# Optimization experiments

Measured on AMD Instinct MI355X. Metric: run time of the kernel, lower is better.

Reference implementation:

```python
import jax, jax.numpy as jnp
import numpy as np
import math

D_MODEL = 32    # channels; expand=1 => d_inner == d_model
D_STATE = 8
D_CONV = 4
DT_RANK = math.ceil(D_MODEL / 16)  # 2


def _layernorm(x, g, b, eps=1e-5):
    m = jnp.mean(x, axis=-1, keepdims=True)
    v = jnp.var(x, axis=-1, keepdims=True)
    return (x - m) * jax.lax.rsqrt(v + eps) * g + b


def _causal_dwconv(x, w, b):
    # x: [B, D, L], w: [D, 1, K] depthwise causal conv (pad K-1 on the left)
    y = jax.lax.conv_general_dilated(
        x, w, window_strides=(1,), padding=[(D_CONV - 1, 0)],
        dimension_numbers=('NCH', 'OIH', 'NCH'),
        feature_group_count=x.shape[1])
    return y + b[None, :, None]


def _ssm_branch(xb, z, conv_w, conv_b, xproj_w, dtproj_w, dtproj_b, A_log, Dp):
    # One mamba_inner (no out_proj) branch. xb, z: [B, D, L]
    Bsz, Dd, L = xb.shape
    u = jax.nn.silu(_causal_dwconv(xb, conv_w, conv_b))              # [B,D,L]
    x_dbl = jnp.einsum('bdl,rd->blr', u, xproj_w)                    # [B,L,R+2N]
    dt = x_dbl[..., :DT_RANK]                                        # [B,L,R]
    Bm = x_dbl[..., DT_RANK:DT_RANK + D_STATE]                       # [B,L,N]
    Cm = x_dbl[..., DT_RANK + D_STATE:]                              # [B,L,N]
    delta = jax.nn.softplus(jnp.einsum('blr,dr->bld', dt, dtproj_w) + dtproj_b)  # [B,L,D]
    A = -jnp.exp(A_log)                                              # [D,N]

    def step(h, inp):
        d_l, u_l, B_l, C_l = inp   # [B,D], [B,D], [B,N], [B,N]
        dA = jnp.exp(d_l[..., None] * A)                             # [B,D,N]
        h = dA * h + (d_l * u_l)[..., None] * B_l[:, None, :]
        y = jnp.einsum('bdn,bn->bd', h, C_l)
        return h, y

    h0 = jnp.zeros((Bsz, Dd, D_STATE), dtype=xb.dtype)
    _, ys = jax.lax.scan(step, h0,
                         (delta.transpose(1, 0, 2), u.transpose(2, 0, 1),
                          Bm.transpose(1, 0, 2), Cm.transpose(1, 0, 2)))
    y = ys.transpose(1, 2, 0)                                        # [B,D,L]
    y = y + Dp[None, :, None] * u
    return y * jax.nn.silu(z)


def _forward(x, w1, b1, ln_g, ln_b, in_proj_w,
             conv_w_f, conv_b_f, xproj_w_f, dtproj_w_f, dtproj_b_f, A_log_f, D_f,
             conv_w_b, conv_b_b, xproj_w_b, dtproj_w_b, dtproj_b_b, A_log_b, D_b,
             norm_g, norm_b, out_proj_w, w2, b2):
    s = jnp.max(x, axis=(2, 3))                                      # AdaptiveMaxPool2d((1,1)) -> [B,L]
    h = s[..., None] * w1[None, None, :, 0] + b1                     # Linear(1, d_model) -> [B,L,D]
    h = _layernorm(h, ln_g, ln_b)
    # Mamba, bimamba v2
    xz = jnp.einsum('bld,ed->bel', h, in_proj_w)                     # [B,2D,L]
    x_f, z_f = jnp.split(xz, 2, axis=1)
    out_f = _ssm_branch(x_f, z_f, conv_w_f, conv_b_f, xproj_w_f,
                        dtproj_w_f, dtproj_b_f, A_log_f, D_f)
    xz_r = jnp.flip(xz, axis=-1)
    x_b, z_b = jnp.split(xz_r, 2, axis=1)
    out_b = _ssm_branch(x_b, z_b, conv_w_b, conv_b_b, xproj_w_b,
                        dtproj_w_b, dtproj_b_b, A_log_b, D_b)
    y = (out_f + jnp.flip(out_b, axis=-1)).transpose(0, 2, 1)        # [B,L,D]
    y = _layernorm(y, norm_g, norm_b) / 2.0                          # use_norm + if_devide_out
    y = jnp.einsum('bld,od->blo', y, out_proj_w)                     # out_proj -> [B,L,D]
    o = jnp.einsum('bld,od->blo', y, w2) + b2                        # Linear(d_model, 1) -> [B,L,1]
    return jax.nn.sigmoid(o)[..., None]                              # [B,L,1,1]


def setup_inputs() -> dict:
    key = jax.random.key(0)
    ks = jax.random.split(key, 16)
    B, Cin, H, W = 16, 128, 256, 256
    D, N, R = D_MODEL, D_STATE, DT_RANK

    def nrm(k, shp, s=0.2):
        return jax.random.normal(k, shp, dtype=jnp.float32) * s

    A_log_init = jnp.log(jnp.arange(1, N + 1, dtype=jnp.float32))[None, :] * jnp.ones((D, 1), jnp.float32)
    return dict(
        x=jax.random.normal(ks[0], (B, Cin, H, W), dtype=jnp.float32),
        w1=nrm(ks[1], (D, 1), 0.5), b1=nrm(ks[2], (D,), 0.1),
        ln_g=jnp.ones((D,), jnp.float32), ln_b=jnp.zeros((D,), jnp.float32),
        in_proj_w=nrm(ks[3], (2 * D, D)),
        conv_w_f=nrm(ks[4], (D, 1, D_CONV)), conv_b_f=nrm(ks[5], (D,), 0.1),
        xproj_w_f=nrm(ks[6], (R + 2 * N, D)),
        dtproj_w_f=nrm(ks[7], (D, R)), dtproj_b_f=nrm(ks[8], (D,), 0.1),
        A_log_f=A_log_init, D_f=jnp.ones((D,), jnp.float32),
        conv_w_b=nrm(ks[9], (D, 1, D_CONV)), conv_b_b=nrm(ks[10], (D,), 0.1),
        xproj_w_b=nrm(ks[11], (R + 2 * N, D)),
        dtproj_w_b=nrm(ks[12], (D, R)), dtproj_b_b=nrm(ks[13], (D,), 0.1),
        A_log_b=A_log_init, D_b=jnp.ones((D,), jnp.float32),
        norm_g=jnp.ones((D,), jnp.float32), norm_b=jnp.zeros((D,), jnp.float32),
        out_proj_w=nrm(ks[14], (D, D)),
        w2=nrm(ks[15], (1, D), 0.5), b2=jnp.zeros((1,), jnp.float32),
    )


def reference(x, w1, b1, ln_g, ln_b, in_proj_w,
              conv_w_f, conv_b_f, xproj_w_f, dtproj_w_f, dtproj_b_f, A_log_f, D_f,
              conv_w_b, conv_b_b, xproj_w_b, dtproj_w_b, dtproj_b_b, A_log_b, D_b,
              norm_g, norm_b, out_proj_w, w2, b2):
    return _forward(x, w1, b1, ln_g, ln_b, in_proj_w,
                    conv_w_f, conv_b_f, xproj_w_f, dtproj_w_f, dtproj_b_f, A_log_f, D_f,
                    conv_w_b, conv_b_b, xproj_w_b, dtproj_w_b, dtproj_b_b, A_log_b, D_b,
                    norm_g, norm_b, out_proj_w, w2, b2)
```

## Files before the change

kernel.cpp:

```cpp
#include <hip/hip_runtime.h>
#include <hip/hip_bf16.h>
#include <math.h>

#define B_SZ 16
#define L_SEQ 128
#define D_M 32
#define N_ST 8
#define HW 65536
#define NROWS (B_SZ * 128)
#define NCHUNK 2

typedef float vfloat4 __attribute__((ext_vector_type(4)));

__device__ float g_part[NROWS * NCHUNK];
__device__ float g_y0[B_SZ * D_M * L_SEQ];
__device__ float g_y1[B_SZ * D_M * L_SEQ];

__device__ __forceinline__ float silu_acc(float x) {
    return x / (1.f + expf(-x));
}
__device__ __forceinline__ float softplusf(float x) {
    return (x > 20.f) ? x : log1pf(expf(x));
}

__device__ __forceinline__ float sum8_dpp(float y) {
    float t;
    t = __int_as_float(__builtin_amdgcn_mov_dpp(__float_as_int(y), 0xB1, 0xF, 0xF, true));
    y += t;
    t = __int_as_float(__builtin_amdgcn_mov_dpp(__float_as_int(y), 0x4E, 0xF, 0xF, true));
    y += t;
    t = __int_as_float(__builtin_amdgcn_mov_dpp(__float_as_int(y), 0x141, 0xF, 0xF, true));
    y += t;
    return y;
}

__global__ __launch_bounds__(256) void kmax(const float* __restrict__ x) {
    const int blk = blockIdx.x;
    const vfloat4* __restrict__ p =
        reinterpret_cast<const vfloat4*>(x) + (size_t)blk * 8192;
    const int t = threadIdx.x;
    float m0 = -INFINITY, m1 = -INFINITY, m2 = -INFINITY, m3 = -INFINITY;
#pragma unroll
    for (int i = 0; i < 8192; i += 1024) {
        vfloat4 v0 = __builtin_nontemporal_load(p + i + t);
        vfloat4 v1 = __builtin_nontemporal_load(p + i + t + 256);
        vfloat4 v2 = __builtin_nontemporal_load(p + i + t + 512);
        vfloat4 v3 = __builtin_nontemporal_load(p + i + t + 768);
        m0 = fmaxf(m0, fmaxf(fmaxf(v0.x, v0.y), fmaxf(v0.z, v0.w)));
        m1 = fmaxf(m1, fmaxf(fmaxf(v1.x, v1.y), fmaxf(v1.z, v1.w)));
        m2 = fmaxf(m2, fmaxf(fmaxf(v2.x, v2.y), fmaxf(v2.z, v2.w)));
        m3 = fmaxf(m3, fmaxf(fmaxf(v3.x, v3.y), fmaxf(v3.z, v3.w)));
    }
    float m = fmaxf(fmaxf(m0, m1), fmaxf(m2, m3));
#pragma unroll
    for (int off = 32; off >= 1; off >>= 1)
        m = fmaxf(m, __shfl_xor(m, off));
    __shared__ float sm[4];
    if ((threadIdx.x & 63) == 0) sm[threadIdx.x >> 6] = m;
    __syncthreads();
    if (threadIdx.x == 0)
        g_part[blk] = fmaxf(fmaxf(sm[0], sm[1]), fmaxf(sm[2], sm[3]));
}

__device__ __forceinline__ float row_max(int row) {
    const int r2 = row * NCHUNK;
    return fmaxf(g_part[r2], g_part[r2 + 1]);
}

__device__ __forceinline__ void compute_h(int row, const float* __restrict__ w1,
                                          const float* __restrict__ b1,
                                          const float* __restrict__ lng,
                                          const float* __restrict__ lnb,
                                          float h[D_M]) {
    const float s = row_max(row);
    float mean = 0.f;
#pragma unroll
    for (int d = 0; d < D_M; d++) { h[d] = s * w1[d] + b1[d]; mean += h[d]; }
    mean *= (1.f / D_M);
    float var = 0.f;
#pragma unroll
    for (int d = 0; d < D_M; d++) { float t = h[d] - mean; var += t * t; }
    var *= (1.f / D_M);
    const float rs = rsqrtf(var + 1e-5f);
#pragma unroll
    for (int d = 0; d < D_M; d++) h[d] = (h[d] - mean) * rs * lng[d] + lnb[d];
}

__global__ __launch_bounds__(512) void kbranch(
    const float* __restrict__ w1,  const float* __restrict__ b1,
    const float* __restrict__ lng, const float* __restrict__ lnb,
    const float* __restrict__ Win,
    const float* __restrict__ cw_f, const float* __restrict__ cb_f,
    const float* __restrict__ xp_f, const float* __restrict__ dtw_f,
    const float* __restrict__ dtb_f, const float* __restrict__ Al_f,
    const float* __restrict__ Dp_f,
    const float* __restrict__ cw_b, const float* __restrict__ cb_b,
    const float* __restrict__ xp_b, const float* __restrict__ dtw_b,
    const float* __restrict__ dtb_b, const float* __restrict__ Al_b,
    const float* __restrict__ Dp_b) {
    const int b = blockIdx.x >> 1;
    const int beta = blockIdx.x & 1;
    const int tid = threadIdx.x;

    const float* cw  = beta ? cw_b  : cw_f;
    const float* cb  = beta ? cb_b  : cb_f;
    const float* xp  = beta ? xp_b  : xp_f;
    const float* dtw = beta ? dtw_b : dtw_f;
    const float* dtb = beta ? dtb_b : dtb_f;
    const float* Al  = beta ? Al_b  : Al_f;
    const float* Dp  = beta ? Dp_b  : Dp_f;
    float* yout = beta ? g_y1 : g_y0;

    __shared__ __align__(16) float S[15360];
    float* sx  = S;
    float* sdl = S;
    float* su  = S + 4352;
    float* sy  = S + 8576;
    float* sdt = S + 12800;
    float* sB  = S + 13056;
    float* sC  = S + 14208;

    const int l = tid & 127;
    const int q = tid >> 7;

    if (tid < 128) sx[(tid >> 2) * 136 + (tid & 3)] = 0.f;
    float h[D_M];
    compute_h(b * L_SEQ + l, w1, b1, lng, lnb, h);

    {
        const int lw = beta ? (127 - l) : l;
#pragma unroll
        for (int k = 0; k < 8; k++) {
            const int e = q * 8 + k;
            float acc = 0.f;
#pragma unroll
            for (int d = 0; d < D_M; d++) acc += h[d] * Win[e * 32 + d];
            sx[e * 136 + 4 + lw] = acc;
        }
    }
    __syncthreads();

    {
        const int d = tid >> 4;
        const int l0 = (tid & 15) * 8;
        const vfloat4* px = reinterpret_cast<const vfloat4*>(sx + d * 136 + l0);
        vfloat4 a0 = px[0], a1 = px[1], a2 = px[2];
        float xv[12] = {a0.x,a0.y,a0.z,a0.w, a1.x,a1.y,a1.z,a1.w, a2.x,a2.y,a2.z,a2.w};
        const float c0 = cw[d*4+0], c1 = cw[d*4+1], c2 = cw[d*4+2], c3 = cw[d*4+3];
        const float cbd = cb[d];
        float uo[8];
#pragma unroll
        for (int j = 0; j < 8; j++) {
            float acc = cbd + c0*xv[j+1] + c1*xv[j+2] + c2*xv[j+3] + c3*xv[j+4];
            uo[j] = silu_acc(acc);
        }
        vfloat4* pu = reinterpret_cast<vfloat4*>(su + d * 132 + l0);
        vfloat4 w0 = {uo[0],uo[1],uo[2],uo[3]}, w1v = {uo[4],uo[5],uo[6],uo[7]};
        pu[0] = w0; pu[1] = w1v;
    }
    __syncthreads();

    {
        float ul[D_M];
#pragma unroll
        for (int d = 0; d < D_M; d++) ul[d] = su[d * 132 + l];
        const int r0 = (q < 3) ? q * 5 : 15;
        const int nr = (q < 3) ? 5 : 3;
        for (int j = 0; j < nr; j++) {
            const int r = r0 + j;
            float acc = 0.f;
#pragma unroll
            for (int d = 0; d < D_M; d++) acc += ul[d] * xp[r * 32 + d];
            if (r < 2)       sdt[l * 2 + r] = acc;
            else if (r < 10) sB[l * 9 + (r - 2)] = acc;
            else             sC[l * 9 + (r - 10)] = acc;
        }
    }
    __syncthreads();

    {
        const float dt0 = sdt[l * 2 + 0], dt1 = sdt[l * 2 + 1];
        const int d0 = q * 8;
#pragma unroll
        for (int j = 0; j < 8; j++) {
            const int d = d0 + j;
            const float t = dt0 * dtw[d * 2 + 0] + dt1 * dtw[d * 2 + 1] + dtb[d];
            sdl[l * 33 + d] = softplusf(t);
        }
    }
    __syncthreads();

    if (tid < 256) {
        const int d = tid >> 3, n = tid & 7;
        const float A = -expf(Al[d * 8 + n]);
        const float Dd = Dp[d];
        float hst = 0.f;
        float dl = sdl[d], ul = su[d * 132], Bv = sB[n], Cv = sC[n];
        for (int ll = 0; ll < L_SEQ; ll++) {
            float dl_n = 0.f, ul_n = 0.f, Bv_n = 0.f, Cv_n = 0.f;
            if (ll < 127) {
                dl_n = sdl[(ll + 1) * 33 + d];
                ul_n = su[d * 132 + ll + 1];
                Bv_n = sB[(ll + 1) * 9 + n];
                Cv_n = sC[(ll + 1) * 9 + n];
            }
            const float dA = expf(dl * A);
            hst = dA * hst + (dl * ul) * Bv;
            const float y = sum8_dpp(hst * Cv);
            if (n == 0) sy[d * 132 + ll] = y + Dd * ul;
            dl = dl_n; ul = ul_n; Bv = Bv_n; Cv = Cv_n;
        }
    }
    __syncthreads();

    for (int i = tid; i < 4096; i += 512) {
        const int d = i >> 7, li = i & 127;
        const int gl = beta ? (127 - li) : li;
        yout[(b * D_M + d) * L_SEQ + gl] = sy[d * 132 + li];
    }
}

__global__ __launch_bounds__(128) void kfinal(
    const float* __restrict__ w1,  const float* __restrict__ b1,
    const float* __restrict__ lng, const float* __restrict__ lnb,
    const float* __restrict__ Win,
    const float* __restrict__ ng,  const float* __restrict__ nb,
    const float* __restrict__ Wout, const float* __restrict__ w2,
    const float* __restrict__ b2,  float* __restrict__ out) {
    const int b = blockIdx.x;
    const int l = threadIdx.x;

    float h[D_M];
    compute_h(b * L_SEQ + l, w1, b1, lng, lnb, h);

    float v[D_M];
#pragma unroll
    for (int d = 0; d < D_M; d++) {
        float z = 0.f;
#pragma unroll
        for (int k = 0; k < D_M; k++) z += h[k] * Win[(32 + d) * 32 + k];
        const float yc = g_y0[(b * D_M + d) * L_SEQ + l] +
                         g_y1[(b * D_M + d) * L_SEQ + l];
        v[d] = yc * silu_acc(z);
    }

    float mean = 0.f;
#pragma unroll
    for (int d = 0; d < D_M; d++) mean += v[d];
    mean *= (1.f / D_M);
    float var = 0.f;
#pragma unroll
    for (int d = 0; d < D_M; d++) { float t = v[d] - mean; var += t * t; }
    var *= (1.f / D_M);
    const float rs = rsqrtf(var + 1e-5f);
#pragma unroll
    for (int d = 0; d < D_M; d++)
        v[d] = ((v[d] - mean) * rs * ng[d] + nb[d]) * 0.5f;

    float acc = 0.f;
    for (int o = 0; o < D_M; o++) {
        float t = 0.f;
#pragma unroll
        for (int d = 0; d < D_M; d++) t += v[d] * Wout[o * 32 + d];
        acc += t * w2[o];
    }
    acc += b2[0];
    out[b * L_SEQ + l] = 1.f / (1.f + expf(-acc));
}

extern "C" void kernel_launch(void* const* d_in, const int* in_sizes, int n_in,
                              void* d_out, int out_size, void* d_ws, size_t ws_size,
                              hipStream_t stream) {
    const float* x        = (const float*)d_in[0];
    const float* w1       = (const float*)d_in[1];
    const float* b1       = (const float*)d_in[2];
    const float* ln_g     = (const float*)d_in[3];
    const float* ln_b     = (const float*)d_in[4];
    const float* in_proj  = (const float*)d_in[5];
    const float* cw_f     = (const float*)d_in[6];
    const float* cb_f     = (const float*)d_in[7];
    const float* xp_f     = (const float*)d_in[8];
    const float* dtw_f    = (const float*)d_in[9];
    const float* dtb_f    = (const float*)d_in[10];
    const float* Al_f     = (const float*)d_in[11];
    const float* Dp_f     = (const float*)d_in[12];
    const float* cw_b     = (const float*)d_in[13];
    const float* cb_b     = (const float*)d_in[14];
    const float* xp_b     = (const float*)d_in[15];
    const float* dtw_b    = (const float*)d_in[16];
    const float* dtb_b    = (const float*)d_in[17];
    const float* Al_b     = (const float*)d_in[18];
    const float* Dp_b     = (const float*)d_in[19];
    const float* norm_g   = (const float*)d_in[20];
    const float* norm_b   = (const float*)d_in[21];
    const float* Wout     = (const float*)d_in[22];
    const float* w2       = (const float*)d_in[23];
    const float* b2       = (const float*)d_in[24];

    kmax<<<NROWS * NCHUNK, 256, 0, stream>>>(x);
    kbranch<<<B_SZ * 2, 512, 0, stream>>>(w1, b1, ln_g, ln_b, in_proj,
                                          cw_f, cb_f, xp_f, dtw_f, dtb_f, Al_f, Dp_f,
                                          cw_b, cb_b, xp_b, dtw_b, dtb_b, Al_b, Dp_b);
    kfinal<<<B_SZ, 128, 0, stream>>>(w1, b1, ln_g, ln_b, in_proj,
                                     norm_g, norm_b, Wout, w2, b2, (float*)d_out);
}
```

Before: 126.4 us.

## Fuse max-reduce, both SSM branches and head into one kernel with tail-block handoff

Replaces the three-kernel pipeline with a single launch where each block reduces one row's max, and the last-arriving block per batch (atomic counter) runs both scan directions and the final projection. This removes two kernel launch boundaries and the global round trip of branch outputs. In exchange both directions are serialized within one block and the large shared allocation may reduce occupancy during the bandwidth-bound reduction.

Result: slower. 225.7 us (+78.6%).

```diff
diff --git a/kernel.cpp b/kernel.cpp
--- a/kernel.cpp
+++ b/kernel.cpp
@@ -5,16 +5,12 @@
 #define B_SZ 16
 #define L_SEQ 128
 #define D_M 32
-#define N_ST 8
 #define HW 65536
-#define NROWS (B_SZ * 128)
-#define NCHUNK 2
 
 typedef float vfloat4 __attribute__((ext_vector_type(4)));
 
-__device__ float g_part[NROWS * NCHUNK];
-__device__ float g_y0[B_SZ * D_M * L_SEQ];
-__device__ float g_y1[B_SZ * D_M * L_SEQ];
+__device__ float g_s[B_SZ * L_SEQ];
+__device__ int   g_cnt[B_SZ];
 
 __device__ __forceinline__ float silu_acc(float x) {
     return x / (1.f + expf(-x));
@@ -34,45 +30,12 @@
     return y;
 }
 
-__global__ __launch_bounds__(256) void kmax(const float* __restrict__ x) {
-    const int blk = blockIdx.x;
-    const vfloat4* __restrict__ p =
-        reinterpret_cast<const vfloat4*>(x) + (size_t)blk * 8192;
-    const int t = threadIdx.x;
-    float m0 = -INFINITY, m1 = -INFINITY, m2 = -INFINITY, m3 = -INFINITY;
-#pragma unroll
-    for (int i = 0; i < 8192; i += 1024) {
-        vfloat4 v0 = __builtin_nontemporal_load(p + i + t);
-        vfloat4 v1 = __builtin_nontemporal_load(p + i + t + 256);
-        vfloat4 v2 = __builtin_nontemporal_load(p + i + t + 512);
-        vfloat4 v3 = __builtin_nontemporal_load(p + i + t + 768);
-        m0 = fmaxf(m0, fmaxf(fmaxf(v0.x, v0.y), fmaxf(v0.z, v0.w)));
-        m1 = fmaxf(m1, fmaxf(fmaxf(v1.x, v1.y), fmaxf(v1.z, v1.w)));
-        m2 = fmaxf(m2, fmaxf(fmaxf(v2.x, v2.y), fmaxf(v2.z, v2.w)));
-        m3 = fmaxf(m3, fmaxf(fmaxf(v3.x, v3.y), fmaxf(v3.z, v3.w)));
-    }
-    float m = fmaxf(fmaxf(m0, m1), fmaxf(m2, m3));
-#pragma unroll
-    for (int off = 32; off >= 1; off >>= 1)
-        m = fmaxf(m, __shfl_xor(m, off));
-    __shared__ float sm[4];
-    if ((threadIdx.x & 63) == 0) sm[threadIdx.x >> 6] = m;
-    __syncthreads();
-    if (threadIdx.x == 0)
-        g_part[blk] = fmaxf(fmaxf(sm[0], sm[1]), fmaxf(sm[2], sm[3]));
-}
-
-__device__ __forceinline__ float row_max(int row) {
-    const int r2 = row * NCHUNK;
-    return fmaxf(g_part[r2], g_part[r2 + 1]);
-}
-
 __device__ __forceinline__ void compute_h(int row, const float* __restrict__ w1,
                                           const float* __restrict__ b1,
                                           const float* __restrict__ lng,
                                           const float* __restrict__ lnb,
                                           float h[D_M]) {
-    const float s = row_max(row);
+    const float s = g_s[row];
     float mean = 0.f;
 #pragma unroll
     for (int d = 0; d < D_M; d++) { h[d] = s * w1[d] + b1[d]; mean += h[d]; }
@@ -86,7 +49,8 @@
     for (int d = 0; d < D_M; d++) h[d] = (h[d] - mean) * rs * lng[d] + lnb[d];
 }
 
-__global__ __launch_bounds__(512) void kbranch(
+__global__ __launch_bounds__(512, 2) void fused(
+    const float* __restrict__ x,
     const float* __restrict__ w1,  const float* __restrict__ b1,
     const float* __restrict__ lng, const float* __restrict__ lnb,
     const float* __restrict__ Win,
@@ -97,175 +61,202 @@
     const float* __restrict__ cw_b, const float* __restrict__ cb_b,
     const float* __restrict__ xp_b, const float* __restrict__ dtw_b,
     const float* __restrict__ dtb_b, const float* __restrict__ Al_b,
-    const float* __restrict__ Dp_b) {
-    const int b = blockIdx.x >> 1;
-    const int beta = blockIdx.x & 1;
-    const int tid = threadIdx.x;
-
-    const float* cw  = beta ? cw_b  : cw_f;
-    const float* cb  = beta ? cb_b  : cb_f;
-    const float* xp  = beta ? xp_b  : xp_f;
-    const float* dtw = beta ? dtw_b : dtw_f;
-    const float* dtb = beta ? dtb_b : dtb_f;
-    const float* Al  = beta ? Al_b  : Al_f;
-    const float* Dp  = beta ? Dp_b  : Dp_f;
-    float* yout = beta ? g_y1 : g_y0;
-
-    __shared__ __align__(16) float S[15360];
-    float* sx  = S;
-    float* sdl = S;
-    float* su  = S + 4352;
-    float* sy  = S + 8576;
-    float* sdt = S + 12800;
-    float* sB  = S + 13056;
-    float* sC  = S + 14208;
-
-    const int l = tid & 127;
-    const int q = tid >> 7;
-
-    if (tid < 128) sx[(tid >> 2) * 136 + (tid & 3)] = 0.f;
-    float h[D_M];
-    compute_h(b * L_SEQ + l, w1, b1, lng, lnb, h);
-
-    {
-        const int lw = beta ? (127 - l) : l;
-#pragma unroll
-        for (int k = 0; k < 8; k++) {
-            const int e = q * 8 + k;
-            float acc = 0.f;
-#pragma unroll
-            for (int d = 0; d < D_M; d++) acc += h[d] * Win[e * 32 + d];
-            sx[e * 136 + 4 + lw] = acc;
-        }
-    }
-    __syncthreads();
-
-    {
-        const int d = tid >> 4;
-        const int l0 = (tid & 15) * 8;
-        const vfloat4* px = reinterpret_cast<const vfloat4*>(sx + d * 136 + l0);
-        vfloat4 a0 = px[0], a1 = px[1], a2 = px[2];
-        float xv[12] = {a0.x,a0.y,a0.z,a0.w, a1.x,a1.y,a1.z,a1.w, a2.x,a2.y,a2.z,a2.w};
-        const float c0 = cw[d*4+0], c1 = cw[d*4+1], c2 = cw[d*4+2], c3 = cw[d*4+3];
-        const float cbd = cb[d];
-        float uo[8];
-#pragma unroll
-        for (int j = 0; j < 8; j++) {
-            float acc = cbd + c0*xv[j+1] + c1*xv[j+2] + c2*xv[j+3] + c3*xv[j+4];
-            uo[j] = silu_acc(acc);
-        }
-        vfloat4* pu = reinterpret_cast<vfloat4*>(su + d * 132 + l0);
-        vfloat4 w0 = {uo[0],uo[1],uo[2],uo[3]}, w1v = {uo[4],uo[5],uo[6],uo[7]};
-        pu[0] = w0; pu[1] = w1v;
-    }
-    __syncthreads();
-
-    {
-        float ul[D_M];
-#pragma unroll
-        for (int d = 0; d < D_M; d++) ul[d] = su[d * 132 + l];
-        const int r0 = (q < 3) ? q * 5 : 15;
-        const int nr = (q < 3) ? 5 : 3;
-        for (int j = 0; j < nr; j++) {
-            const int r = r0 + j;
-            float acc = 0.f;
-#pragma unroll
-            for (int d = 0; d < D_M; d++) acc += ul[d] * xp[r * 32 + d];
-            if (r < 2)       sdt[l * 2 + r] = acc;
-            else if (r < 10) sB[l * 9 + (r - 2)] = acc;
-            else             sC[l * 9 + (r - 10)] = acc;
-        }
-    }
-    __syncthreads();
-
-    {
-        const float dt0 = sdt[l * 2 + 0], dt1 = sdt[l * 2 + 1];
-        const int d0 = q * 8;
-#pragma unroll
-        for (int j = 0; j < 8; j++) {
-            const int d = d0 + j;
-            const float t = dt0 * dtw[d * 2 + 0] + dt1 * dtw[d * 2 + 1] + dtb[d];
-            sdl[l * 33 + d] = softplusf(t);
-        }
-    }
-    __syncthreads();
-
-    if (tid < 256) {
-        const int d = tid >> 3, n = tid & 7;
-        const float A = -expf(Al[d * 8 + n]);
-        const float Dd = Dp[d];
-        float hst = 0.f;
-        float dl = sdl[d], ul = su[d * 132], Bv = sB[n], Cv = sC[n];
-        for (int ll = 0; ll < L_SEQ; ll++) {
-            float dl_n = 0.f, ul_n = 0.f, Bv_n = 0.f, Cv_n = 0.f;
-            if (ll < 127) {
-                dl_n = sdl[(ll + 1) * 33 + d];
-                ul_n = su[d * 132 + ll + 1];
-                Bv_n = sB[(ll + 1) * 9 + n];
-                Cv_n = sC[(ll + 1) * 9 + n];
-            }
-            const float dA = expf(dl * A);
-            hst = dA * hst + (dl * ul) * Bv;
-            const float y = sum8_dpp(hst * Cv);
-            if (n == 0) sy[d * 132 + ll] = y + Dd * ul;
-            dl = dl_n; ul = ul_n; Bv = Bv_n; Cv = Cv_n;
-        }
-    }
-    __syncthreads();
-
-    for (int i = tid; i < 4096; i += 512) {
-        const int d = i >> 7, li = i & 127;
-        const int gl = beta ? (127 - li) : li;
-        yout[(b * D_M + d) * L_SEQ + gl] = sy[d * 132 + li];
-    }
-}
-
-__global__ __launch_bounds__(128) void kfinal(
-    const float* __restrict__ w1,  const float* __restrict__ b1,
-    const float* __restrict__ lng, const float* __restrict__ lnb,
-    const float* __restrict__ Win,
+    const float* __restrict__ Dp_b,
     const float* __restrict__ ng,  const float* __restrict__ nb,
     const float* __restrict__ Wout, const float* __restrict__ w2,
     const float* __restrict__ b2,  float* __restrict__ out) {
-    const int b = blockIdx.x;
-    const int l = threadIdx.x;
+    const int row = blockIdx.x;
+    const int b   = row >> 7;
+    const int tid = threadIdx.x;
+
+    __shared__ __align__(16) float S[19584];
+    __shared__ float s_m[8];
+    __shared__ int s_flag;
+    float* sy0 = S;
+    float* sy1 = S + 4224;
+    float* sx  = S + 8448;
+    float* sdl = S + 8448;
+    float* su  = S + 12800;
+    float* sdt = S + 17024;
+    float* sB  = S + 17280;
+    float* sC  = S + 18432;
+
+    {
+        const vfloat4* __restrict__ p =
+            reinterpret_cast<const vfloat4*>(x) + (size_t)row * (HW / 4);
+        float m0 = -INFINITY, m1 = -INFINITY, m2 = -INFINITY, m3 = -INFINITY;
+#pragma unroll
+        for (int i = 0; i < 16384; i += 2048) {
+            vfloat4 v0 = __builtin_nontemporal_load(p + i + tid);
+            vfloat4 v1 = __builtin_nontemporal_load(p + i + tid + 512);
+            vfloat4 v2 = __builtin_nontemporal_load(p + i + tid + 1024);
+            vfloat4 v3 = __builtin_nontemporal_load(p + i + tid + 1536);
+            m0 = fmaxf(m0, fmaxf(fmaxf(v0.x, v0.y), fmaxf(v0.z, v0.w)));
+            m1 = fmaxf(m1, fmaxf(fmaxf(v1.x, v1.y), fmaxf(v1.z, v1.w)));
+            m2 = fmaxf(m2, fmaxf(fmaxf(v2.x, v2.y), fmaxf(v2.z, v2.w)));
+            m3 = fmaxf(m3, fmaxf(fmaxf(v3.x, v3.y), fmaxf(v3.z, v3.w)));
+        }
+        float m = fmaxf(fmaxf(m0, m1), fmaxf(m2, m3));
+#pragma unroll
+        for (int off = 32; off >= 1; off >>= 1)
+            m = fmaxf(m, __shfl_xor(m, off));
+        if ((tid & 63) == 0) s_m[tid >> 6] = m;
+        __syncthreads();
+        if (tid == 0) {
+            float mm = s_m[0];
+#pragma unroll
+            for (int w = 1; w < 8; w++) mm = fmaxf(mm, s_m[w]);
+            g_s[row] = mm;
+            __threadfence();
+            const int old = atomicAdd(&g_cnt[b], 1);
+            const int isTail = (old == 127);
+            if (isTail) {
+                atomicExch(&g_cnt[b], 0);
+                __threadfence();
+            }
+            s_flag = isTail;
+        }
+        __syncthreads();
+        if (!s_flag) return;
+    }
+
+    const int l = tid & 127;
+    const int q = tid >> 7;
 
     float h[D_M];
     compute_h(b * L_SEQ + l, w1, b1, lng, lnb, h);
 
-    float v[D_M];
-#pragma unroll
-    for (int d = 0; d < D_M; d++) {
-        float z = 0.f;
-#pragma unroll
-        for (int k = 0; k < D_M; k++) z += h[k] * Win[(32 + d) * 32 + k];
-        const float yc = g_y0[(b * D_M + d) * L_SEQ + l] +
-                         g_y1[(b * D_M + d) * L_SEQ + l];
-        v[d] = yc * silu_acc(z);
+    for (int dir = 0; dir < 2; ++dir) {
+        const float* cw  = dir ? cw_b  : cw_f;
+        const float* cb  = dir ? cb_b  : cb_f;
+        const float* xp  = dir ? xp_b  : xp_f;
+        const float* dtw = dir ? dtw_b : dtw_f;
+        const float* dtb = dir ? dtb_b : dtb_f;
+        const float* Al  = dir ? Al_b  : Al_f;
+        const float* Dp  = dir ? Dp_b  : Dp_f;
+        float* syd = dir ? sy1 : sy0;
+
+        if (tid < 128) sx[(tid >> 2) * 136 + (tid & 3)] = 0.f;
+        {
+            const int lw = dir ? (127 - l) : l;
+#pragma unroll
+            for (int k = 0; k < 8; k++) {
+                const int e = q * 8 + k;
+                float acc = 0.f;
+#pragma unroll
+                for (int d = 0; d < D_M; d++) acc += h[d] * Win[e * 32 + d];
+                sx[e * 136 + 4 + lw] = acc;
+            }
+        }
+        __syncthreads();
+
+        {
+            const int d = tid >> 4;
+            const int l0 = (tid & 15) * 8;
+            const vfloat4* px = reinterpret_cast<const vfloat4*>(sx + d * 136 + l0);
+            vfloat4 a0 = px[0], a1 = px[1], a2 = px[2];
+            float xv[12] = {a0.x,a0.y,a0.z,a0.w, a1.x,a1.y,a1.z,a1.w, a2.x,a2.y,a2.z,a2.w};
+            const float c0 = cw[d*4+0], c1 = cw[d*4+1], c2 = cw[d*4+2], c3 = cw[d*4+3];
+            const float cbd = cb[d];
+            float uo[8];
+#pragma unroll
+            for (int j = 0; j < 8; j++) {
+                float acc = cbd + c0*xv[j+1] + c1*xv[j+2] + c2*xv[j+3] + c3*xv[j+4];
+                uo[j] = silu_acc(acc);
+            }
+            vfloat4* pu = reinterpret_cast<vfloat4*>(su + d * 132 + l0);
+            vfloat4 u0 = {uo[0],uo[1],uo[2],uo[3]}, u1 = {uo[4],uo[5],uo[6],uo[7]};
+            pu[0] = u0; pu[1] = u1;
+        }
+        __syncthreads();
+
+        {
+            float ul[D_M];
+#pragma unroll
+            for (int d = 0; d < D_M; d++) ul[d] = su[d * 132 + l];
+            const int r0 = (q < 3) ? q * 5 : 15;
+            const int nr = (q < 3) ? 5 : 3;
+            for (int j = 0; j < nr; j++) {
+                const int r = r0 + j;
+                float acc = 0.f;
+#pragma unroll
+                for (int d = 0; d < D_M; d++) acc += ul[d] * xp[r * 32 + d];
+                if (r < 2)       sdt[l * 2 + r] = acc;
+                else if (r < 10) sB[l * 9 + (r - 2)] = acc;
+                else             sC[l * 9 + (r - 10)] = acc;
+            }
+        }
+        __syncthreads();
+
+        {
+            const float dt0 = sdt[l * 2 + 0], dt1 = sdt[l * 2 + 1];
+            const int d0 = q * 8;
+#pragma unroll
+            for (int j = 0; j < 8; j++) {
+                const int d = d0 + j;
+                const float t = dt0 * dtw[d * 2 + 0] + dt1 * dtw[d * 2 + 1] + dtb[d];
+                sdl[l * 33 + d] = softplusf(t);
+            }
+        }
+        __syncthreads();
+
+        if (tid < 256) {
+            const int d = tid >> 3, n = tid & 7;
+            const float A = -expf(Al[d * 8 + n]);
+            const float Dd = Dp[d];
+            float hst = 0.f;
+            float dl = sdl[d], ul = su[d * 132], Bv = sB[n], Cv = sC[n];
+            for (int ll = 0; ll < L_SEQ; ll++) {
+                float dl_n = 0.f, ul_n = 0.f, Bv_n = 0.f, Cv_n = 0.f;
+                if (ll < 127) {
+                    dl_n = sdl[(ll + 1) * 33 + d];
+                    ul_n = su[d * 132 + ll + 1];
+                    Bv_n = sB[(ll + 1) * 9 + n];
+                    Cv_n = sC[(ll + 1) * 9 + n];
+                }
+                const float dA = expf(dl * A);
+                hst = dA * hst + (dl * ul) * Bv;
+                const float y = sum8_dpp(hst * Cv);
+                if (n == 0) syd[d * 132 + ll] = y + Dd * ul;
+                dl = dl_n; ul = ul_n; Bv = Bv_n; Cv = Cv_n;
+            }
+        }
+        __syncthreads();
     }
 
-    float mean = 0.f;
-#pragma unroll
-    for (int d = 0; d < D_M; d++) mean += v[d];
-    mean *= (1.f / D_M);
-    float var = 0.f;
-#pragma unroll
-    for (int d = 0; d < D_M; d++) { float t = v[d] - mean; var += t * t; }
-    var *= (1.f / D_M);
-    const float rs = rsqrtf(var + 1e-5f);
-#pragma unroll
-    for (int d = 0; d < D_M; d++)
-        v[d] = ((v[d] - mean) * rs * ng[d] + nb[d]) * 0.5f;
-
-    float acc = 0.f;
-    for (int o = 0; o < D_M; o++) {
-        float t = 0.f;
-#pragma unroll
-        for (int d = 0; d < D_M; d++) t += v[d] * Wout[o * 32 + d];
-        acc += t * w2[o];
+    if (tid < 128) {
+        float v[D_M];
+#pragma unroll
+        for (int d = 0; d < D_M; d++) {
+            float z = 0.f;
+#pragma unroll
+            for (int k = 0; k < D_M; k++) z += h[k] * Win[(32 + d) * 32 + k];
+            const float yc = sy0[d * 132 + l] + sy1[d * 132 + (127 - l)];
+            v[d] = yc * silu_acc(z);
+        }
+        float mean = 0.f;
+#pragma unroll
+        for (int d = 0; d < D_M; d++) mean += v[d];
+        mean *= (1.f / D_M);
+        float var = 0.f;
+#pragma unroll
+        for (int d = 0; d < D_M; d++) { float t = v[d] - mean; var += t * t; }
+        var *= (1.f / D_M);
+        const float rs = rsqrtf(var + 1e-5f);
+#pragma unroll
+        for (int d = 0; d < D_M; d++)
+            v[d] = ((v[d] - mean) * rs * ng[d] + nb[d]) * 0.5f;
+
+        float acc = 0.f;
+        for (int o = 0; o < D_M; o++) {
+            float t = 0.f;
+#pragma unroll
+            for (int d = 0; d < D_M; d++) t += v[d] * Wout[o * 32 + d];
+            acc += t * w2[o];
+        }
+        acc += b2[0];
+        out[b * L_SEQ + l] = 1.f / (1.f + expf(-acc));
     }
-    acc += b2[0];
-    out[b * L_SEQ + l] = 1.f / (1.f + expf(-acc));
 }
 
 extern "C" void kernel_launch(void* const* d_in, const int* in_sizes, int n_in,
@@ -297,10 +288,9 @@
     const float* w2       = (const float*)d_in[23];
     const float* b2       = (const float*)d_in[24];
 
-    kmax<<<NROWS * NCHUNK, 256, 0, stream>>>(x);
-    kbranch<<<B_SZ * 2, 512, 0, stream>>>(w1, b1, ln_g, ln_b, in_proj,
-                                          cw_f, cb_f, xp_f, dtw_f, dtb_f, Al_f, Dp_f,
-                                          cw_b, cb_b, xp_b, dtw_b, dtb_b, Al_b, Dp_b);
-    kfinal<<<B_SZ, 128, 0, stream>>>(w1, b1, ln_g, ln_b, in_proj,
-                                     norm_g, norm_b, Wout, w2, b2, (float*)d_out);
-}
+    fused<<<B_SZ * L_SEQ, 512, 0, stream>>>(
+        x, w1, b1, ln_g, ln_b, in_proj,
+        cw_f, cb_f, xp_f, dtw_f, dtb_f, Al_f, Dp_f,
+        cw_b, cb_b, xp_b, dtw_b, dtb_b, Al_b, Dp_b,
+        norm_g, norm_b, Wout, w2, b2, (float*)d_out);
+}
```

## Fuse final epilogue into branch kernel via last-block-done atomic counter

Applied to the files above, without the earlier changes.

Merges the separate final kernel into the branch kernel. Each batch's two direction blocks increment an atomic counter, and the second block to finish reads the other direction's output from global memory and runs the gated layernorm, out projection and sigmoid. The goal is to remove one kernel launch and the global round trip for its own direction. It also adds a warm-up pass that touches every weight array so later reads hit cache. The cost is an atomic, threadfences and serial epilogue work in one block per batch.

After: 128.2 us. About the same (+1.4%).

```diff
diff --git a/kernel.cpp b/kernel.cpp
--- a/kernel.cpp
+++ b/kernel.cpp
@@ -5,7 +5,6 @@
 #define B_SZ 16
 #define L_SEQ 128
 #define D_M 32
-#define N_ST 8
 #define HW 65536
 #define NROWS (B_SZ * 128)
 #define NCHUNK 2
@@ -13,8 +12,8 @@
 typedef float vfloat4 __attribute__((ext_vector_type(4)));
 
 __device__ float g_part[NROWS * NCHUNK];
-__device__ float g_y0[B_SZ * D_M * L_SEQ];
-__device__ float g_y1[B_SZ * D_M * L_SEQ];
+__device__ float g_y[2][B_SZ * D_M * L_SEQ];
+__device__ int   g_done[B_SZ];
 
 __device__ __forceinline__ float silu_acc(float x) {
     return x / (1.f + expf(-x));
@@ -34,6 +33,36 @@
     return y;
 }
 
+__device__ __forceinline__ float row_max(int row) {
+    const int r2 = row * NCHUNK;
+    return fmaxf(g_part[r2], g_part[r2 + 1]);
+}
+
+__device__ __forceinline__ void compute_h(int row, const float* __restrict__ w1,
+                                          const float* __restrict__ b1,
+                                          const float* __restrict__ lng,
+                                          const float* __restrict__ lnb,
+                                          float h[D_M]) {
+    const float s = row_max(row);
+    float mean = 0.f;
+#pragma unroll
+    for (int d = 0; d < D_M; d++) { h[d] = s * w1[d] + b1[d]; mean += h[d]; }
+    mean *= (1.f / D_M);
+    float var = 0.f;
+#pragma unroll
+    for (int d = 0; d < D_M; d++) { float t = h[d] - mean; var += t * t; }
+    var *= (1.f / D_M);
+    const float rs = rsqrtf(var + 1e-5f);
+#pragma unroll
+    for (int d = 0; d < D_M; d++) h[d] = (h[d] - mean) * rs * lng[d] + lnb[d];
+}
+
+__device__ __forceinline__ float warm_arr(const float* __restrict__ a, int n, int tid) {
+    float s = 0.f;
+    for (int i = tid; i < n; i += 512) s += a[i];
+    return s;
+}
+
 __global__ __launch_bounds__(256) void kmax(const float* __restrict__ x) {
     const int blk = blockIdx.x;
     const vfloat4* __restrict__ p =
@@ -62,31 +91,7 @@
         g_part[blk] = fmaxf(fmaxf(sm[0], sm[1]), fmaxf(sm[2], sm[3]));
 }
 
-__device__ __forceinline__ float row_max(int row) {
-    const int r2 = row * NCHUNK;
-    return fmaxf(g_part[r2], g_part[r2 + 1]);
-}
-
-__device__ __forceinline__ void compute_h(int row, const float* __restrict__ w1,
-                                          const float* __restrict__ b1,
-                                          const float* __restrict__ lng,
-                                          const float* __restrict__ lnb,
-                                          float h[D_M]) {
-    const float s = row_max(row);
-    float mean = 0.f;
-#pragma unroll
-    for (int d = 0; d < D_M; d++) { h[d] = s * w1[d] + b1[d]; mean += h[d]; }
-    mean *= (1.f / D_M);
-    float var = 0.f;
-#pragma unroll
-    for (int d = 0; d < D_M; d++) { float t = h[d] - mean; var += t * t; }
-    var *= (1.f / D_M);
-    const float rs = rsqrtf(var + 1e-5f);
-#pragma unroll
-    for (int d = 0; d < D_M; d++) h[d] = (h[d] - mean) * rs * lng[d] + lnb[d];
-}
-
-__global__ __launch_bounds__(512) void kbranch(
+__global__ __launch_bounds__(512) void ktail(
     const float* __restrict__ w1,  const float* __restrict__ b1,
     const float* __restrict__ lng, const float* __restrict__ lnb,
     const float* __restrict__ Win,
@@ -97,21 +102,39 @@
     const float* __restrict__ cw_b, const float* __restrict__ cb_b,
     const float* __restrict__ xp_b, const float* __restrict__ dtw_b,
     const float* __restrict__ dtb_b, const float* __restrict__ Al_b,
-    const float* __restrict__ Dp_b) {
-    const int b = blockIdx.x >> 1;
-    const int beta = blockIdx.x & 1;
+    const float* __restrict__ Dp_b,
+    const float* __restrict__ ng,  const float* __restrict__ nb,
+    const float* __restrict__ Wout, const float* __restrict__ w2,
+    const float* __restrict__ b2,  float* __restrict__ out) {
+    const int b   = blockIdx.x >> 1;
+    const int dir = blockIdx.x & 1;
     const int tid = threadIdx.x;
 
-    const float* cw  = beta ? cw_b  : cw_f;
-    const float* cb  = beta ? cb_b  : cb_f;
-    const float* xp  = beta ? xp_b  : xp_f;
-    const float* dtw = beta ? dtw_b : dtw_f;
-    const float* dtb = beta ? dtb_b : dtb_f;
-    const float* Al  = beta ? Al_b  : Al_f;
-    const float* Dp  = beta ? Dp_b  : Dp_f;
-    float* yout = beta ? g_y1 : g_y0;
+    const float* cw  = dir ? cw_b  : cw_f;
+    const float* cb  = dir ? cb_b  : cb_f;
+    const float* xp  = dir ? xp_b  : xp_f;
+    const float* dtw = dir ? dtw_b : dtw_f;
+    const float* dtb = dir ? dtb_b : dtb_f;
+    const float* Al  = dir ? Al_b  : Al_f;
+    const float* Dp  = dir ? Dp_b  : Dp_f;
+
+    {
+        float ws = 0.f;
+        ws += warm_arr(w1, 32, tid)   + warm_arr(b1, 32, tid);
+        ws += warm_arr(lng, 32, tid)  + warm_arr(lnb, 32, tid);
+        ws += warm_arr(Win, 2048, tid);
+        ws += warm_arr(cw, 128, tid)  + warm_arr(cb, 32, tid);
+        ws += warm_arr(xp, 576, tid);
+        ws += warm_arr(dtw, 64, tid)  + warm_arr(dtb, 32, tid);
+        ws += warm_arr(Al, 256, tid)  + warm_arr(Dp, 32, tid);
+        ws += warm_arr(ng, 32, tid)   + warm_arr(nb, 32, tid);
+        ws += warm_arr(Wout, 1024, tid) + warm_arr(w2, 32, tid);
+        ws += warm_arr(b2, 1, tid);
+        asm volatile("" :: "v"(ws));
+    }
 
     __shared__ __align__(16) float S[15360];
+    __shared__ int s_flag;
     float* sx  = S;
     float* sdl = S;
     float* su  = S + 4352;
@@ -128,7 +151,7 @@
     compute_h(b * L_SEQ + l, w1, b1, lng, lnb, h);
 
     {
-        const int lw = beta ? (127 - l) : l;
+        const int lw = dir ? (127 - l) : l;
 #pragma unroll
         for (int k = 0; k < 8; k++) {
             const int e = q * 8 + k;
@@ -155,8 +178,8 @@
             uo[j] = silu_acc(acc);
         }
         vfloat4* pu = reinterpret_cast<vfloat4*>(su + d * 132 + l0);
-        vfloat4 w0 = {uo[0],uo[1],uo[2],uo[3]}, w1v = {uo[4],uo[5],uo[6],uo[7]};
-        pu[0] = w0; pu[1] = w1v;
+        vfloat4 u0 = {uo[0],uo[1],uo[2],uo[3]}, u1 = {uo[4],uo[5],uo[6],uo[7]};
+        pu[0] = u0; pu[1] = u1;
     }
     __syncthreads();
 
@@ -215,57 +238,59 @@
 
     for (int i = tid; i < 4096; i += 512) {
         const int d = i >> 7, li = i & 127;
-        const int gl = beta ? (127 - li) : li;
-        yout[(b * D_M + d) * L_SEQ + gl] = sy[d * 132 + li];
-    }
-}
-
-__global__ __launch_bounds__(128) void kfinal(
-    const float* __restrict__ w1,  const float* __restrict__ b1,
-    const float* __restrict__ lng, const float* __restrict__ lnb,
-    const float* __restrict__ Win,
-    const float* __restrict__ ng,  const float* __restrict__ nb,
-    const float* __restrict__ Wout, const float* __restrict__ w2,
-    const float* __restrict__ b2,  float* __restrict__ out) {
-    const int b = blockIdx.x;
-    const int l = threadIdx.x;
-
-    float h[D_M];
-    compute_h(b * L_SEQ + l, w1, b1, lng, lnb, h);
-
-    float v[D_M];
-#pragma unroll
-    for (int d = 0; d < D_M; d++) {
-        float z = 0.f;
-#pragma unroll
-        for (int k = 0; k < D_M; k++) z += h[k] * Win[(32 + d) * 32 + k];
-        const float yc = g_y0[(b * D_M + d) * L_SEQ + l] +
-                         g_y1[(b * D_M + d) * L_SEQ + l];
-        v[d] = yc * silu_acc(z);
-    }
-
-    float mean = 0.f;
-#pragma unroll
-    for (int d = 0; d < D_M; d++) mean += v[d];
-    mean *= (1.f / D_M);
-    float var = 0.f;
-#pragma unroll
-    for (int d = 0; d < D_M; d++) { float t = v[d] - mean; var += t * t; }
-    var *= (1.f / D_M);
-    const float rs = rsqrtf(var + 1e-5f);
-#pragma unroll
-    for (int d = 0; d < D_M; d++)
-        v[d] = ((v[d] - mean) * rs * ng[d] + nb[d]) * 0.5f;
-
-    float acc = 0.f;
-    for (int o = 0; o < D_M; o++) {
-        float t = 0.f;
-#pragma unroll
-        for (int d = 0; d < D_M; d++) t += v[d] * Wout[o * 32 + d];
-        acc += t * w2[o];
-    }
-    acc += b2[0];
-    out[b * L_SEQ + l] = 1.f / (1.f + expf(-acc));
+        const int gl = dir ? (127 - li) : li;
+        g_y[dir][(b * D_M + d) * L_SEQ + gl] = sy[d * 132 + li];
+    }
+    __syncthreads();
+
+    if (tid == 0) {
+        __threadfence();
+        const int old = atomicAdd(&g_done[b], 1);
+        const int win = (old == 1);
+        if (win) {
+            atomicExch(&g_done[b], 0);
+            __threadfence();
+        }
+        s_flag = win;
+    }
+    __syncthreads();
+    if (!s_flag) return;
+
+    if (tid < 128) {
+        const float* yo = g_y[1 - dir];
+        float v[D_M];
+#pragma unroll
+        for (int d = 0; d < D_M; d++) {
+            float z = 0.f;
+#pragma unroll
+            for (int k = 0; k < D_M; k++) z += h[k] * Win[(32 + d) * 32 + k];
+            const float own = sy[d * 132 + (dir ? (127 - l) : l)];
+            const float yc  = own + yo[(b * D_M + d) * L_SEQ + l];
+            v[d] = yc * silu_acc(z);
+        }
+        float mean = 0.f;
+#pragma unroll
+        for (int d = 0; d < D_M; d++) mean += v[d];
+        mean *= (1.f / D_M);
+        float var = 0.f;
+#pragma unroll
+        for (int d = 0; d < D_M; d++) { float t = v[d] - mean; var += t * t; }
+        var *= (1.f / D_M);
+        const float rs = rsqrtf(var + 1e-5f);
+#pragma unroll
+        for (int d = 0; d < D_M; d++)
+            v[d] = ((v[d] - mean) * rs * ng[d] + nb[d]) * 0.5f;
+
+        float acc = 0.f;
+        for (int o = 0; o < D_M; o++) {
+            float t = 0.f;
+#pragma unroll
+            for (int d = 0; d < D_M; d++) t += v[d] * Wout[o * 32 + d];
+            acc += t * w2[o];
+        }
+        acc += b2[0];
+        out[b * L_SEQ + l] = 1.f / (1.f + expf(-acc));
+    }
 }
 
 extern "C" void kernel_launch(void* const* d_in, const int* in_sizes, int n_in,
@@ -298,9 +323,8 @@
     const float* b2       = (const float*)d_in[24];
 
     kmax<<<NROWS * NCHUNK, 256, 0, stream>>>(x);
-    kbranch<<<B_SZ * 2, 512, 0, stream>>>(w1, b1, ln_g, ln_b, in_proj,
-                                          cw_f, cb_f, xp_f, dtw_f, dtb_f, Al_f, Dp_f,
-                                          cw_b, cb_b, xp_b, dtw_b, dtb_b, Al_b, Dp_b);
-    kfinal<<<B_SZ, 128, 0, stream>>>(w1, b1, ln_g, ln_b, in_proj,
-                                     norm_g, norm_b, Wout, w2, b2, (float*)d_out);
-}
+    ktail<<<B_SZ * 2, 512, 0, stream>>>(w1, b1, ln_g, ln_b, in_proj,
+                                        cw_f, cb_f, xp_f, dtw_f, dtb_f, Al_f, Dp_f,
+                                        cw_b, cb_b, xp_b, dtw_b, dtb_b, Al_b, Dp_b,
+                                        norm_g, norm_b, Wout, w2, b2, (float*)d_out);
+}
```
